# Kernel tuning notes

Hardware: AMD Instinct MI355X
Metric: run time of the kernel (lower is better)

## Reference

```python
import jax, jax.numpy as jnp
import numpy as np

NUM_KERNELS = 6
ALPHA = 0.5
DIL = 9
FEAT = 4
DELTA_V = 0.5
DELTA_D = 1.5
EMB_W = 0.25
MAX_LABELS = 16


def setup_inputs() -> dict:
    key = jax.random.key(0)
    k1, k2, k3, k4, k5 = jax.random.split(key, 5)
    B, H, W = 8, 640, 640
    pred = jax.random.normal(k1, (B, NUM_KERNELS + FEAT, H, W), dtype=jnp.float32)
    gt_text = (jax.random.uniform(k2, (B, 1, H, W)) < 0.3).astype(jnp.float32)
    gt_kernels = (jax.random.uniform(k3, (B, NUM_KERNELS - 1, H, W)) < 0.2).astype(jnp.float32)
    training_mask = (jax.random.uniform(k4, (B, 1, H, W)) > 0.05).astype(jnp.float32)
    gt_instance = jax.random.randint(k5, (B, H, W), 0, MAX_LABELS, dtype=jnp.int32)
    return {"pred": pred, "gt_text": gt_text, "gt_kernels": gt_kernels,
            "training_mask": training_mask, "gt_instance": gt_instance}


def _dice(inp, tgt, msk, eps=1e-6):
    # inp/tgt/msk: [N, HW]; returns mean over N of (1 - 2*I/U)
    inp = inp * msk
    tgt = tgt * msk
    inter = (inp * tgt).sum(1)
    union = (inp ** 2).sum(1) + (tgt ** 2).sum(1) + eps
    return (1.0 - 2.0 * inter / union).mean()


def _ohem(pred, gt, tm, ratio=3):
    # Vectorized OHEM: keep all positives + top-(3*n_pos) hardest negatives per sample.
    B = gt.shape[0]
    p = pred.reshape(B, -1)
    g = gt.reshape(B, -1)
    m = tm.reshape(B, -1)
    pos = (g > 0.5) & (m > 0.5)
    neg = (g <= 0.5) & (m > 0.5)
    n_pos = pos.sum(1)
    n_neg = jnp.minimum(ratio * n_pos, neg.sum(1))
    score = jnp.where(neg, p, -jnp.inf)
    # rank[i,j] = position of element j in descending order of score[i]
    rank = jnp.argsort(jnp.argsort(-score, axis=1), axis=1)
    mask = pos | (neg & (rank < n_neg[:, None]))
    return mask.astype(pred.dtype).reshape(gt.shape)


def _emb_sample(emb, gt, tm):
    # emb: [D,H,W], gt: [H,W] int, tm: [H,W]
    D = emb.shape[0]
    e = emb.reshape(D, -1).T                       # [HW, D]
    g = gt.reshape(-1)
    valid = tm.reshape(-1) > 0
    ids = jnp.where(valid, g, MAX_LABELS)          # invalid pixels -> dump segment
    ones = valid.astype(e.dtype)
    counts = jax.ops.segment_sum(ones, ids, num_segments=MAX_LABELS + 1)[:MAX_LABELS]
    sums = jax.ops.segment_sum(e * ones[:, None], ids, num_segments=MAX_LABELS + 1)[:MAX_LABELS]
    present = counts > 0
    n = present.sum()
    nf = n.astype(e.dtype)
    means = sums / jnp.maximum(counts, 1.0)[:, None]   # [L, D]
    # variance term: per-pixel distance to own cluster mean
    own = means[g]                                     # [HW, D]
    d = jnp.sqrt(((e - own) ** 2).sum(1) + 1e-12)
    cv = jnp.maximum(d - DELTA_V, 0.0) ** 2
    per = jax.ops.segment_sum(cv * ones, ids, num_segments=MAX_LABELS + 1)[:MAX_LABELS]
    per = per / jnp.maximum(counts, 1.0)
    lv = jnp.where(present, per, 0.0).sum() / jnp.maximum(nf, 1.0)
    # distance term: pairwise over present cluster means (unordered pairs i<j)
    diff = means[:, None, :] - means[None, :, :]
    pd = jnp.sqrt((diff ** 2).sum(-1) + 1e-12)
    iu = jnp.arange(MAX_LABELS)
    pm = present[:, None] & present[None, :] & (iu[:, None] < iu[None, :])
    ld = jnp.where(pm, jnp.maximum(2.0 * DELTA_D - pd, 0.0) ** 2, 0.0).sum()
    ld = ld / jnp.maximum(nf * (nf - 1.0), 1.0)
    # regularization: mean norm of present cluster means
    lr = jnp.where(present, jnp.sqrt((means ** 2).sum(1) + 1e-12), 0.0).sum() / jnp.maximum(nf, 1.0)
    act = (n > 1).astype(e.dtype)   # skip samples with <=1 instance (matches `continue`)
    return act * lv, act * ld, act * lr


def reference(pred, gt_text, gt_kernels, training_mask, gt_instance):
    B = pred.shape[0]
    gt_t = gt_text[:, 0]
    tm = training_mask[:, 0]
    # text branch: sigmoid -> 9x9 max-pool dilation -> OHEM dice
    prob = jax.nn.sigmoid(pred[:, 0])
    pad = DIL // 2
    dil = jax.lax.reduce_window(prob, -jnp.inf, jax.lax.max,
                                (1, DIL, DIL), (1, 1, 1),
                                [(0, 0), (pad, pad), (pad, pad)])
    ohem = jax.lax.stop_gradient(_ohem(dil, gt_t, tm, ratio=3))
    loss_text = _dice(dil.reshape(B, -1), gt_t.reshape(B, -1), ohem.reshape(B, -1))
    # kernel branch: mean over (B, K) equals sum_k dice_k / K
    K = NUM_KERNELS - 1
    pk = jax.nn.sigmoid(pred[:, 1:NUM_KERNELS]).reshape(B * K, -1)
    gk = gt_kernels.reshape(B * K, -1)
    mk = jnp.broadcast_to(tm[:, None], (B, K) + tm.shape[1:]).reshape(B * K, -1)
    loss_kernels = _dice(pk, gk, mk)
    # embedding clustering loss
    pred_emb = pred[:, NUM_KERNELS:]
    lv, ld, lr = jax.vmap(_emb_sample)(pred_emb, gt_instance, tm)
    loss_emb = EMB_W * (lv.sum() + ld.sum() + 0.001 * (lr.sum() / B))
    loss = loss_kernels + ALPHA * loss_text + loss_emb
    return loss, loss_text, loss_kernels, loss_emb
```

## Files before the change

### kernel.cpp

```cpp
#include <hip/hip_runtime.h>
#include <math.h>

#define BB 8
#define HH 640
#define WW 640
#define HWN (HH*WW)
#define CC 10
#define KCH 5
#define DD 4
#define LL 16
#define NBINS 256
#define ETILE 1024

#define NDIL   800
#define NDICEB 2048
#define EGX    64
#define EGRID  (EGX * BB)

#define WS_OHEM      0
#define WS_HCNT      64
#define WS_HS2       (WS_HCNT + BB*NBINS)
#define WS_KERN      (WS_HS2 + BB*NBINS)
#define WS_ECNT      (WS_KERN + 120)
#define WS_ESUM      (WS_ECNT + BB*LL)
#define WS_ECV       (WS_ESUM + BB*LL*DD)
#define WS_BAR       (WS_ECV + BB)
#define WS_ZERO_END  (WS_BAR + 4)

typedef short bf16x8 __attribute__((ext_vector_type(8)));
typedef float f32x4  __attribute__((ext_vector_type(4)));

__device__ __forceinline__ float sigm(float x) { return 1.f / (1.f + __expf(-x)); }

__device__ __forceinline__ float wave_red(float v) {
    #pragma unroll
    for (int o = 32; o > 0; o >>= 1) v += __shfl_down(v, o);
    return v;
}

__device__ __forceinline__ unsigned short f2bf(float x) {
    return (unsigned short)((__float_as_uint(x) + 0x8000u) >> 16);
}

__device__ __forceinline__ float4 ld4g(const float* __restrict__ p, int row, int cb) {
    float4 v;
    if (row < 0 || row >= HH) { v.x = v.y = v.z = v.w = -INFINITY; return v; }
    const float* rp = p + (size_t)row * WW;
    if (cb >= 0 && cb <= WW - 4) return *(const float4*)(rp + cb);
    v.x = ((unsigned)(cb + 0) < (unsigned)WW) ? rp[cb + 0] : -INFINITY;
    v.y = ((unsigned)(cb + 1) < (unsigned)WW) ? rp[cb + 1] : -INFINITY;
    v.z = ((unsigned)(cb + 2) < (unsigned)WW) ? rp[cb + 2] : -INFINITY;
    v.w = ((unsigned)(cb + 3) < (unsigned)WW) ? rp[cb + 3] : -INFINITY;
    return v;
}

__global__ __launch_bounds__(256) void k_front(
    const float* __restrict__ pred, const float* __restrict__ gt_t,
    const float* __restrict__ gtk,  const float* __restrict__ tm,
    float* __restrict__ ws)
{
    __shared__ float smem[72 * 65 + 4 * NBINS + 8];
    const int tid = threadIdx.x;
    const int blk = blockIdx.x;

    if (blk < NDIL) {
        float* hmax = smem;
        float* hcnt = smem + 72 * 65;
        float* hs2  = hcnt + 2 * NBINS;
        float* red  = hs2 + 2 * NBINS;
        const int b   = blk / 100;
        const int rem = blk - b * 100;
        const int y0  = (rem / 10) * 64;
        const int x0  = (rem - (rem / 10) * 10) * 64;
        const float* p0 = pred + (size_t)b * CC * HWN;

        for (int i = tid; i < 4 * NBINS; i += 256) hcnt[i] = 0.f;
        if (tid < 8) red[tid] = 0.f;

        for (int i = tid; i < 72 * 16; i += 256) {
            int r = i >> 4, g = i & 15;
            int gr = y0 + r - 4;
            int cb = x0 + 4 * g - 4;
            float4 A  = ld4g(p0, gr, cb);
            float4 Bv = ld4g(p0, gr, cb + 4);
            float4 Cv = ld4g(p0, gr, cb + 8);
            float s3 = A.w;
            float s2 = fmaxf(A.z, s3);
            float s1 = fmaxf(A.y, s2);
            float s0 = fmaxf(A.x, s1);
            float mid = fmaxf(fmaxf(Bv.x, Bv.y), fmaxf(Bv.z, Bv.w));
            float q0 = Cv.x;
            float q1 = fmaxf(q0, Cv.y);
            float q2 = fmaxf(q1, Cv.z);
            float q3 = fmaxf(q2, Cv.w);
            int c = 4 * g;
            hmax[r * 65 + c + 0] = fmaxf(fmaxf(s0, mid), q0);
            hmax[r * 65 + c + 1] = fmaxf(fmaxf(s1, mid), q1);
            hmax[r * 65 + c + 2] = fmaxf(fmaxf(s2, mid), q2);
            hmax[r * 65 + c + 3] = fmaxf(fmaxf(s3, mid), q3);
        }
        __syncthreads();

        const int c  = tid & 63;
        const int rb = tid >> 6;
        const int hc = (tid >> 7) * NBINS;
        float c_pos = 0.f, s_pos = 0.f, s_pos2 = 0.f, c_neg = 0.f, s_neg2 = 0.f;
        #pragma unroll
        for (int k = 0; k < 16; k++) {
            int r = rb * 16 + k;
            float m = hmax[r * 65 + c];
            #pragma unroll
            for (int j = 1; j < 9; j++) m = fmaxf(m, hmax[(r + j) * 65 + c]);
            float dil = sigm(m);
            size_t gidx = (size_t)b * HWN + (size_t)(y0 + r) * WW + (x0 + c);
            float g = gt_t[gidx], mv = tm[gidx];
            if (mv > 0.5f) {
                if (g > 0.5f) { c_pos += 1.f; s_pos += dil; s_pos2 += dil * dil; }
                else {
                    c_neg += 1.f; s_neg2 += dil * dil;
                    int bin = (int)((m + 8.f) * 16.f);
                    bin = min(max(bin, 0), NBINS - 1);
                    atomicAdd(&hcnt[hc + bin], 1.f);
                    atomicAdd(&hs2[hc + bin], dil * dil);
                }
            }
        }
        c_pos = wave_red(c_pos); s_pos = wave_red(s_pos); s_pos2 = wave_red(s_pos2);
        c_neg = wave_red(c_neg); s_neg2 = wave_red(s_neg2);
        if ((tid & 63) == 0) {
            atomicAdd(&red[0], c_pos);  atomicAdd(&red[1], s_pos);
            atomicAdd(&red[2], s_pos2); atomicAdd(&red[3], c_neg);
            atomicAdd(&red[4], s_neg2);
        }
        __syncthreads();
        float* oh = ws + WS_OHEM + b * 8;
        if (tid < 5) atomicAdd(&oh[tid], red[tid]);
        float* gh_c = ws + WS_HCNT + b * NBINS;
        float* gh_s = ws + WS_HS2  + b * NBINS;
        for (int i = tid; i < NBINS; i += 256) {
            float sc = hcnt[i] + hcnt[NBINS + i];
            if (sc != 0.f) {
                atomicAdd(&gh_c[i], sc);
                atomicAdd(&gh_s[i], hs2[i] + hs2[NBINS + i]);
            }
        }
    } else {
        const int d  = blk - NDIL;
        const int b  = d >> 8;
        const int xb = d & 255;
        const float* pb = pred + ((size_t)b * CC + 1) * HWN;
        const float* gb = gtk + (size_t)b * KCH * HWN;
        const float4* m = (const float4*)(tm + (size_t)b * HWN);
        const int nv = HWN / 4;
        float i1[KCH], i2[KCH], i3[KCH];
        #pragma unroll
        for (int c = 0; c < KCH; c++) { i1[c] = 0.f; i2[c] = 0.f; i3[c] = 0.f; }

        for (int j = xb * 256 + tid; j < nv; j += 256 * 256) {
            float4 mv = m[j];
            #pragma unroll
            for (int c = 0; c < KCH; c++) {
                float4 pv = ((const float4*)(pb + (size_t)c * HWN))[j];
                float4 gv = ((const float4*)(gb + (size_t)c * HWN))[j];
                float s0 = sigm(pv.x), s1 = sigm(pv.y), s2 = sigm(pv.z), s3 = sigm(pv.w);
                i1[c] += s0*gv.x*mv.x + s1*gv.y*mv.y + s2*gv.z*mv.z + s3*gv.w*mv.w;
                i2[c] += s0*s0*mv.x + s1*s1*mv.y + s2*s2*mv.z + s3*s3*mv.w;
                i3[c] += gv.x*mv.x + gv.y*mv.y + gv.z*mv.z + gv.w*mv.w;
            }
        }

        float* sred = smem;
        const int wv = tid >> 6;
        #pragma unroll
        for (int c = 0; c < KCH; c++) {
            float r1 = wave_red(i1[c]);
            float r2 = wave_red(i2[c]);
            float r3 = wave_red(i3[c]);
            if ((tid & 63) == 0) {
                sred[wv*15 + c*3+0] = r1; sred[wv*15 + c*3+1] = r2; sred[wv*15 + c*3+2] = r3;
            }
        }
        __syncthreads();
        if (tid < 15) {
            float s = sred[tid] + sred[15 + tid] + sred[30 + tid] + sred[45 + tid];
            int c = tid / 3, jj = tid - c * 3;
            atomicAdd(&ws[WS_KERN + (b * KCH + c) * 3 + jj], s);
        }
    }
}

__global__ __launch_bounds__(256, 3) void k_emb(
    const float* __restrict__ pred, const int* __restrict__ inst,
    const float* __restrict__ tm, float* __restrict__ ws)
{
    const int b = blockIdx.y;
    __shared__ unsigned short chs[4][ETILE + 16];
    __shared__ unsigned int   labv[ETILE];
    __shared__ float          merge[4 * 80];
    const int tid  = threadIdx.x;
    const int wave = tid >> 6, lane = tid & 63;
    const int q = lane >> 4, n = lane & 15;
    const float* e0  = pred + ((size_t)b * CC + 6) * HWN;
    const float* tmb = tm + (size_t)b * HWN;
    const int*   ib  = inst + (size_t)b * HWN;

    const bool isch = (n >= 1 && n <= 4);
    const int  cn   = isch ? (n - 1) : 0;

    f32x4 acc = {0.f, 0.f, 0.f, 0.f};

    for (int t0 = blockIdx.x * ETILE; t0 < HWN; t0 += EGX * ETILE) {
        {
            int p = t0 + tid * 4;
            float4 T = *(const float4*)(tmb + p);
            int4   L = *(const int4*)(ib + p);
            #pragma unroll
            for (int c = 0; c < 4; c++) {
                float4 V = *(const float4*)(e0 + (size_t)c * HWN + p);
                unsigned short* dst = &chs[c][tid * 4];
                dst[0] = f2bf(V.x); dst[1] = f2bf(V.y);
                dst[2] = f2bf(V.z); dst[3] = f2bf(V.w);
            }
            uint4 lv;
            lv.x = (T.x > 0.f) ? (unsigned)L.x : 255u;
            lv.y = (T.y > 0.f) ? (unsigned)L.y : 255u;
            lv.z = (T.z > 0.f) ? (unsigned)L.z : 255u;
            lv.w = (T.w > 0.f) ? (unsigned)L.w : 255u;
            *(uint4*)&labv[tid * 4] = lv;
        }
        __syncthreads();

        for (int c2 = wave; c2 < ETILE / 32; c2 += 4) {
            const int base = c2 * 32 + q * 8;
            uint4 La = *(const uint4*)&labv[base];
            uint4 Lb = *(const uint4*)&labv[base + 4];
            union { unsigned short u[8]; bf16x8 v; } A_;
            const unsigned un = (unsigned)n;
            A_.u[0] = (La.x == un) ? 0x3F80 : 0;
            A_.u[1] = (La.y == un) ? 0x3F80 : 0;
            A_.u[2] = (La.z == un) ? 0x3F80 : 0;
            A_.u[3] = (La.w == un) ? 0x3F80 : 0;
            A_.u[4] = (Lb.x == un) ? 0x3F80 : 0;
            A_.u[5] = (Lb.y == un) ? 0x3F80 : 0;
            A_.u[6] = (Lb.z == un) ? 0x3F80 : 0;
            A_.u[7] = (Lb.w == un) ? 0x3F80 : 0;
            bf16x8 Bf;
            if (isch) {
                Bf = *(const bf16x8*)&chs[cn][base];
            } else if (n == 0) {
                #pragma unroll
                for (int j = 0; j < 8; j++) Bf[j] = (short)0x3F80;
            } else {
                #pragma unroll
                for (int j = 0; j < 8; j++) Bf[j] = 0;
            }
            acc = __builtin_amdgcn_mfma_f32_16x16x32_bf16(A_.v, Bf, acc, 0, 0, 0);
        }
        __syncthreads();
    }

    if (n <= 4) {
        #pragma unroll
        for (int r = 0; r < 4; r++)
            merge[wave * 80 + (q * 4 + r) * 5 + n] = acc[r];
    }
    __syncthreads();
    if (tid < 80) {
        float s = merge[tid] + merge[80 + tid] + merge[160 + tid] + merge[240 + tid];
        int l = tid / 5, c = tid - l * 5;
        if (c == 0) atomicAdd(&ws[WS_ECNT + b * LL + l], s);
        else        atomicAdd(&ws[WS_ESUM + b * LL * DD + l * DD + (c - 1)], s);
    }
    __syncthreads();

    int* bar = (int*)(ws + WS_BAR);
    if (tid == 0) {
        __threadfence();
        __hip_atomic_fetch_add(bar, 1, __ATOMIC_ACQ_REL, __HIP_MEMORY_SCOPE_AGENT);
        while (__hip_atomic_load(bar, __ATOMIC_ACQUIRE, __HIP_MEMORY_SCOPE_AGENT) < EGRID) {
            __builtin_amdgcn_s_sleep(8);
        }
    }
    __syncthreads();

    __shared__ float mn[LL * DD];
    __shared__ float invc[LL];
    if (tid < LL) {
        float c = ws[WS_ECNT + b * LL + tid];
        invc[tid] = 1.f / fmaxf(c, 1.f);
    }
    __syncthreads();
    if (tid < LL * DD) {
        int l = tid >> 2;
        mn[tid] = ws[WS_ESUM + b * LL * DD + tid] * invc[l];
    }
    __syncthreads();

    const float4* v0p = (const float4*)e0;
    const float4* v1p = (const float4*)(e0 + HWN);
    const float4* v2p = (const float4*)(e0 + 2 * HWN);
    const float4* v3p = (const float4*)(e0 + 3 * HWN);
    const float4* tmv = (const float4*)tmb;
    const int4*   iv  = (const int4*)ib;

    float vacc = 0.f;
    const int nv = HWN / 4;
    for (int j = blockIdx.x * 256 + tid; j < nv; j += EGX * 256) {
        float4 a0 = v0p[j], a1 = v1p[j], a2 = v2p[j], a3 = v3p[j];
        float4 t = tmv[j];
        int4 li = iv[j];
        float ex[4] = {a0.x, a0.y, a0.z, a0.w};
        float ey[4] = {a1.x, a1.y, a1.z, a1.w};
        float ez[4] = {a2.x, a2.y, a2.z, a2.w};
        float ew[4] = {a3.x, a3.y, a3.z, a3.w};
        int   lb[4] = {li.x, li.y, li.z, li.w};
        float tv[4] = {t.x, t.y, t.z, t.w};
        #pragma unroll
        for (int qq = 0; qq < 4; qq++) {
            int l = lb[qq];
            float d0 = ex[qq] - mn[l * DD + 0];
            float d1 = ey[qq] - mn[l * DD + 1];
            float d2 = ez[qq] - mn[l * DD + 2];
            float d3 = ew[qq] - mn[l * DD + 3];
            float dd = sqrtf(d0*d0 + d1*d1 + d2*d2 + d3*d3 + 1e-12f);
            float tt = fmaxf(dd - 0.5f, 0.f);
            float w = (tv[qq] > 0.f) ? invc[l] : 0.f;
            vacc += w * tt * tt;
        }
    }

    vacc = wave_red(vacc);
    __shared__ float sred[4];
    if ((tid & 63) == 0) sred[wave] = vacc;
    __syncthreads();
    if (tid == 0)
        atomicAdd(&ws[WS_ECV + b], sred[0] + sred[1] + sred[2] + sred[3]);
}

__global__ __launch_bounds__(256) void k_final(const float* __restrict__ ws, float* __restrict__ out)
{
    __shared__ float mn[BB][LL][DD];
    __shared__ float pres[BB][LL];
    __shared__ float nfa[BB], lda[BB], lra[BB];
    __shared__ float s_text[BB];
    __shared__ float s_kern[40];
    __shared__ float s_lv[BB], s_ld[BB], s_lr[BB];
    const int tid = threadIdx.x;
    if (tid < BB) { nfa[tid] = 0.f; lda[tid] = 0.f; lra[tid] = 0.f; }
    __syncthreads();
    if (tid < BB * LL) {
        int b = tid >> 4, l = tid & 15;
        float c = ws[WS_ECNT + b * LL + l];
        float inv = 1.f / fmaxf(c, 1.f);
        #pragma unroll
        for (int d = 0; d < DD; d++)
            mn[b][l][d] = ws[WS_ESUM + b * LL * DD + l * DD + d] * inv;
        float p = (c > 0.f) ? 1.f : 0.f;
        pres[b][l] = p;
        atomicAdd(&nfa[b], p);
    }
    __syncthreads();
    for (int t = tid; t < BB * 120; t += 256) {
        int b = t / 120, idx = t - b * 120, ii = 0;
        while (idx >= (LL - 1 - ii)) { idx -= (LL - 1 - ii); ii++; }
        int jj = ii + 1 + idx;
        if (pres[b][ii] > 0.f && pres[b][jj] > 0.f) {
            float s = 1e-12f;
            #pragma unroll
            for (int d = 0; d < DD; d++) {
                float df = mn[b][ii][d] - mn[b][jj][d]; s += df * df;
            }
            float tt = fmaxf(3.0f - sqrtf(s), 0.f);
            if (tt > 0.f) atomicAdd(&lda[b], tt * tt);
        }
    }
    if (tid < BB * LL) {
        int b = tid >> 4, l = tid & 15;
        if (pres[b][l] > 0.f) {
            float s = 1e-12f;
            #pragma unroll
            for (int d = 0; d < DD; d++) s += mn[b][l][d] * mn[b][l][d];
            atomicAdd(&lra[b], sqrtf(s));
        }
    }
    __syncthreads();
    if (tid < BB) {
        const float* o = ws + WS_OHEM + tid * 8;
        float npos = o[0], spos = o[1], spos2 = o[2], nnegt = o[3], sneg2t = o[4];
        float nneg = fminf(3.f * npos, nnegt);
        float ssel;
        if (nneg >= nnegt) ssel = sneg2t;
        else {
            const float* hcn = ws + WS_HCNT + tid * NBINS;
            const float* hs = ws + WS_HS2  + tid * NBINS;
            float acc = 0.f; ssel = 0.f;
            for (int i = NBINS - 1; i >= 0; i--) {
                float c = hcn[i];
                if (c <= 0.f) continue;
                if (acc + c <= nneg) { ssel += hs[i]; acc += c; }
                else { float r = nneg - acc; ssel += r * (hs[i] / c); break; }
            }
        }
        float uni = spos2 + ssel + npos + 1e-6f;
        s_text[tid] = 1.f - 2.f * spos / uni;

        float nf  = nfa[tid];
        float act = (nf > 1.f) ? 1.f : 0.f;
        s_lv[tid] = act * ws[WS_ECV + tid] / fmaxf(nf, 1.f);
        s_ld[tid] = act * lda[tid] / fmaxf(nf * (nf - 1.f), 1.f);
        s_lr[tid] = act * lra[tid] / fmaxf(nf, 1.f);
    }
    if (tid < 40) {
        const float* kk = ws + WS_KERN + tid * 3;
        s_kern[tid] = 1.f - 2.f * kk[0] / (kk[1] + kk[2] + 1e-6f);
    }
    __syncthreads();
    if (tid == 0) {
        float lt = 0.f; for (int i = 0; i < BB; i++) lt += s_text[i]; lt /= (float)BB;
        float lk = 0.f; for (int i = 0; i < 40; i++) lk += s_kern[i]; lk /= 40.f;
        float lvs = 0.f, lds_ = 0.f, lrs = 0.f;
        for (int i = 0; i < BB; i++) { lvs += s_lv[i]; lds_ += s_ld[i]; lrs += s_lr[i]; }
        float lemb = 0.25f * (lvs + lds_ + 0.001f * (lrs / (float)BB));
        out[0] = lk + 0.5f * lt + lemb;
        out[1] = lt;
        out[2] = lk;
        out[3] = lemb;
    }
}

extern "C" void kernel_launch(void* const* d_in, const int* in_sizes, int n_in,
                              void* d_out, int out_size, void* d_ws, size_t ws_size,
                              hipStream_t stream)
{
    (void)in_sizes; (void)n_in; (void)out_size; (void)ws_size;
    const float* pred = (const float*)d_in[0];
    const float* gt_t = (const float*)d_in[1];
    const float* gtk  = (const float*)d_in[2];
    const float* tm   = (const float*)d_in[3];
    const int*   inst = (const int*)d_in[4];
    float* out = (float*)d_out;
    float* ws  = (float*)d_ws;

    hipMemsetAsync(d_ws, 0, WS_ZERO_END * sizeof(float), stream);

    k_front<<<NDIL + NDICEB, 256, 0, stream>>>(pred, gt_t, gtk, tm, ws);
    k_emb<<<dim3(EGX, BB), 256, 0, stream>>>(pred, inst, tm, ws);
    k_final<<<1, 256, 0, stream>>>(ws, out);
}
```

Before: 363.5 us.

## Split embedding kernel at grid barrier into two launches with larger grids

Replaces the software grid-wide spin barrier inside the embedding kernel with a kernel boundary: the first kernel accumulates per-label counts and sums, and the second computes the variance term. Because the barrier is gone, each phase can use its own larger grid (100 and 160 blocks per batch instead of 64), which adds parallelism. The cost is one extra kernel launch, plus a second pass that rereads the embedding inputs in a separate kernel.

```diff
diff --git a/kernel.cpp b/kernel.cpp
--- a/kernel.cpp
+++ b/kernel.cpp
@@ -14,8 +14,6 @@
 
 #define NDIL   800
 #define NDICEB 2048
-#define EGX    64
-#define EGRID  (EGX * BB)
 
 #define WS_OHEM      0
 #define WS_HCNT      64
@@ -24,8 +22,7 @@
 #define WS_ECNT      (WS_KERN + 120)
 #define WS_ESUM      (WS_ECNT + BB*LL)
 #define WS_ECV       (WS_ESUM + BB*LL*DD)
-#define WS_BAR       (WS_ECV + BB)
-#define WS_ZERO_END  (WS_BAR + 4)
+#define WS_ZERO_END  (WS_ECV + BB)
 
 typedef short bf16x8 __attribute__((ext_vector_type(8)));
 typedef float f32x4  __attribute__((ext_vector_type(4)));
@@ -189,7 +186,7 @@
     }
 }
 
-__global__ __launch_bounds__(256, 3) void k_emb(
+__global__ __launch_bounds__(256) void k_emb1(
     const float* __restrict__ pred, const int* __restrict__ inst,
     const float* __restrict__ tm, float* __restrict__ ws)
 {
@@ -209,7 +206,7 @@
 
     f32x4 acc = {0.f, 0.f, 0.f, 0.f};
 
-    for (int t0 = blockIdx.x * ETILE; t0 < HWN; t0 += EGX * ETILE) {
+    for (int t0 = blockIdx.x * ETILE; t0 < HWN; t0 += gridDim.x * ETILE) {
         {
             int p = t0 + tid * 4;
             float4 T = *(const float4*)(tmb + p);
@@ -271,18 +268,14 @@
         if (c == 0) atomicAdd(&ws[WS_ECNT + b * LL + l], s);
         else        atomicAdd(&ws[WS_ESUM + b * LL * DD + l * DD + (c - 1)], s);
     }
-    __syncthreads();
-
-    int* bar = (int*)(ws + WS_BAR);
-    if (tid == 0) {
-        __threadfence();
-        __hip_atomic_fetch_add(bar, 1, __ATOMIC_ACQ_REL, __HIP_MEMORY_SCOPE_AGENT);
-        while (__hip_atomic_load(bar, __ATOMIC_ACQUIRE, __HIP_MEMORY_SCOPE_AGENT) < EGRID) {
-            __builtin_amdgcn_s_sleep(8);
-        }
-    }
-    __syncthreads();
-
+}
+
+__global__ __launch_bounds__(256) void k_emb2(
+    const float* __restrict__ pred, const int* __restrict__ inst,
+    const float* __restrict__ tm, float* __restrict__ ws)
+{
+    const int b = blockIdx.y;
+    const int tid = threadIdx.x;
     __shared__ float mn[LL * DD];
     __shared__ float invc[LL];
     if (tid < LL) {
@@ -296,16 +289,17 @@
     }
     __syncthreads();
 
+    const float* e0 = pred + ((size_t)b * CC + 6) * HWN;
     const float4* v0p = (const float4*)e0;
     const float4* v1p = (const float4*)(e0 + HWN);
     const float4* v2p = (const float4*)(e0 + 2 * HWN);
     const float4* v3p = (const float4*)(e0 + 3 * HWN);
-    const float4* tmv = (const float4*)tmb;
-    const int4*   iv  = (const int4*)ib;
-
-    float vacc = 0.f;
+    const float4* tmv = (const float4*)(tm + (size_t)b * HWN);
+    const int4*   iv  = (const int4*)(inst + (size_t)b * HWN);
+
+    float acc = 0.f;
     const int nv = HWN / 4;
-    for (int j = blockIdx.x * 256 + tid; j < nv; j += EGX * 256) {
+    for (int j = blockIdx.x * 256 + tid; j < nv; j += gridDim.x * 256) {
         float4 a0 = v0p[j], a1 = v1p[j], a2 = v2p[j], a3 = v3p[j];
         float4 t = tmv[j];
         int4 li = iv[j];
@@ -325,13 +319,14 @@
             float dd = sqrtf(d0*d0 + d1*d1 + d2*d2 + d3*d3 + 1e-12f);
             float tt = fmaxf(dd - 0.5f, 0.f);
             float w = (tv[qq] > 0.f) ? invc[l] : 0.f;
-            vacc += w * tt * tt;
-        }
-    }
-
-    vacc = wave_red(vacc);
+            acc += w * tt * tt;
+        }
+    }
+
+    acc = wave_red(acc);
     __shared__ float sred[4];
-    if ((tid & 63) == 0) sred[wave] = vacc;
+    const int wv = tid >> 6;
+    if ((tid & 63) == 0) sred[wv] = acc;
     __syncthreads();
     if (tid == 0)
         atomicAdd(&ws[WS_ECV + b], sred[0] + sred[1] + sred[2] + sred[3]);
@@ -444,6 +439,7 @@
     hipMemsetAsync(d_ws, 0, WS_ZERO_END * sizeof(float), stream);
 
     k_front<<<NDIL + NDICEB, 256, 0, stream>>>(pred, gt_t, gtk, tm, ws);
-    k_emb<<<dim3(EGX, BB), 256, 0, stream>>>(pred, inst, tm, ws);
+    k_emb1<<<dim3(100, BB), 256, 0, stream>>>(pred, inst, tm, ws);
+    k_emb2<<<dim3(160, BB), 256, 0, stream>>>(pred, inst, tm, ws);
     k_final<<<1, 256, 0, stream>>>(ws, out);
 }
```

New measurement: 311.6 us. -14.3%, faster.
